# Optimization experiments

Measured on AMD Instinct MI355X. Metric: run time of the kernel, lower is better.

## Reference

```python
import jax, jax.numpy as jnp
import numpy as np

N = 8192      # nodes
D = 256       # feature dim
GAMMA = 10.0
EPS = 1e-6
DIAG_FILL = -1e-6
# std = 0 in DGM.__init__ default -> the normal(mean=0, std=0) noise is exactly zero, so it is omitted.


def _embed(x, W, edges):
    # minimal message-passing embed_f: h = relu(xW + sum_{(s,d) in E} (xW)[s] -> d)
    h = x @ W
    agg = jax.ops.segment_sum(h[edges[0]], edges[1], num_segments=N)
    return jax.nn.relu(h + agg)


def _cdist(x):
    # pairwise euclidean distance, [N, N]
    sq = jnp.sum(x * x, axis=-1)
    d2 = sq[:, None] + sq[None, :] - 2.0 * (x @ x.T)
    return jnp.sqrt(jnp.clip(d2, 0.0))


def _layernorm(z, gamma, beta):
    # scalar-affine LayerNorm with unbiased std (torch x.std default ddof=1)
    mean = jnp.mean(z, axis=-1, keepdims=True)
    std = jnp.std(z, axis=-1, ddof=1, keepdims=True)
    return gamma * (z - mean) / (std + EPS) + beta


def _entmax15(z):
    # 1.5-entmax over last axis (Peters et al. 2019, exact sort-based algorithm)
    z = z / 2.0
    z = z - jnp.max(z, axis=-1, keepdims=True)
    zs = -jnp.sort(-z, axis=-1)                      # descending sort per row
    k = jnp.arange(1, z.shape[-1] + 1, dtype=z.dtype)
    mean = jnp.cumsum(zs, axis=-1) / k
    meansq = jnp.cumsum(zs * zs, axis=-1) / k
    ss = k * (meansq - mean * mean)
    delta = (1.0 - ss) / k
    tau = mean - jnp.sqrt(jnp.clip(delta, 0.0))
    support = jnp.sum(tau <= zs, axis=-1)            # support size per row
    tau_star = jnp.take_along_axis(tau, (support - 1)[..., None], axis=-1)
    p = jnp.clip(z - tau_star, 0.0)
    return p * p


def setup_inputs() -> dict:
    key = jax.random.key(0)
    k1, k2, k3 = jax.random.split(key, 3)
    x = jax.random.normal(k1, (N, D), dtype=jnp.float32)
    edges = jax.random.randint(k2, (2, 262144), 0, N)
    W = jax.random.normal(k3, (D, D), dtype=jnp.float32) * (1.0 / np.sqrt(D))
    gamma = jnp.full((1,), GAMMA, dtype=jnp.float32)
    beta = jnp.zeros((1,), dtype=jnp.float32)
    return {"x": x, "W": W, "gamma": gamma, "beta": beta, "edges": edges}


def reference(x, W, gamma, beta, edges):
    h = _embed(x, W, edges)                          # [N, D]
    probs = -_cdist(h)                               # [N, N]
    zn = _layernorm(probs, gamma, beta)
    idx = jnp.arange(N)
    zn = zn.at[idx, idx].set(DIAG_FILL)              # fill_diagonal_(-1e-6)
    vprobs = _entmax15(zn)                           # [N, N]
    res = (((vprobs + vprobs.T) * 0.5) > 0).astype(jnp.int32)
    logprobs = jnp.sum(res, axis=1)
    # NOTE: torch returns res.nonzero().t_() (data-dependent shape); we return the
    # equivalent dense adjacency `res` to stay jit-compatible.
    return h, res, logprobs
```

## Files before the change

kernel.cpp:

```cpp
#include <hip/hip_runtime.h>

#define N_NODES 8192
#define NMASK 8191
#define DIMF 256
#define LN_EPS 1e-6f
#define DIAG_Z (-5e-7f)
#define QSCALE 256.0f
#define QINV (1.0f / 256.0f)
#define LDA 40
#define WBS 66

typedef float f32x4 __attribute__((ext_vector_type(4)));
typedef unsigned short ushort8v __attribute__((ext_vector_type(8)));
typedef unsigned short ushort4v __attribute__((ext_vector_type(4)));
typedef short short8v __attribute__((ext_vector_type(8)));

__device__ __forceinline__ unsigned short f2bf(float f) {
  unsigned int u = __float_as_uint(f);
  u = (u + 0x7FFFu + ((u >> 16) & 1u)) >> 16;
  return (unsigned short)u;
}
__device__ __forceinline__ float bf2f(unsigned short s) {
  return __uint_as_float(((unsigned int)s) << 16);
}

__global__ void DGM_22857815949798_kernel() {}

__global__ __launch_bounds__(256) void DGM_22857815949798_dtp(const unsigned short* __restrict__ W16,
                                                              int hint, int* __restrict__ flag) {
  __shared__ float red[4];
  const int t = threadIdx.x;
  if (hint == 0 || hint == 1) { if (t == 0) flag[0] = hint; return; }
  float m = 0.f;
  for (int i = t; i < 2048; i += 256) {
    float v = fabsf(bf2f(W16[i]));
    if (!(v < 1e6f)) v = 1e6f;
    m += v;
  }
#pragma unroll
  for (int o = 32; o; o >>= 1) m += __shfl_down(m, o);
  if ((t & 63) == 0) red[t >> 6] = m;
  __syncthreads();
  if (t == 0) flag[0] = ((red[0] + red[1] + red[2] + red[3]) * (1.0f / 2048.0f) < 10.0f) ? 1 : 0;
}

__global__ __launch_bounds__(256) void DGM_22857815949798_init(int* deg, int* cursor) {
  int i = blockIdx.x * 256 + threadIdx.x;
  if (i < N_NODES) { deg[i] = 0; cursor[i] = 0; }
}

__global__ __launch_bounds__(256) void DGM_22857815949798_e1(const void* __restrict__ xv,
                                                             const void* __restrict__ Wv,
                                                             const int* __restrict__ flag,
                                                             float* __restrict__ h0) {
  __shared__ float xs[4][DIMF];
  const int bf = *flag;
  const int t = threadIdx.x;
  const int r0 = blockIdx.x * 4;
#pragma unroll
  for (int r = 0; r < 4; ++r) {
    size_t idx = (size_t)(r0 + r) * DIMF + t;
    xs[r][t] = bf ? bf2f(((const unsigned short*)xv)[idx]) : ((const float*)xv)[idx];
  }
  __syncthreads();
  float a0 = 0.f, a1 = 0.f, a2 = 0.f, a3 = 0.f;
  for (int k = 0; k < DIMF; ++k) {
    size_t wi = (size_t)k * DIMF + t;
    float w = bf ? bf2f(((const unsigned short*)Wv)[wi]) : ((const float*)Wv)[wi];
    a0 = fmaf(xs[0][k], w, a0);
    a1 = fmaf(xs[1][k], w, a1);
    a2 = fmaf(xs[2][k], w, a2);
    a3 = fmaf(xs[3][k], w, a3);
  }
  h0[(size_t)(r0 + 0) * DIMF + t] = a0;
  h0[(size_t)(r0 + 1) * DIMF + t] = a1;
  h0[(size_t)(r0 + 2) * DIMF + t] = a2;
  h0[(size_t)(r0 + 3) * DIMF + t] = a3;
}

__global__ __launch_bounds__(256) void DGM_22857815949798_deg(const int* __restrict__ dst,
                                                              int* __restrict__ deg, int E) {
  int e = blockIdx.x * 256 + threadIdx.x;
  if (e < E) atomicAdd(&deg[dst[e] & NMASK], 1);
}

__global__ __launch_bounds__(256) void DGM_22857815949798_scan(const int* __restrict__ deg,
                                                               int* __restrict__ off) {
  __shared__ int part[256];
  const int t = threadIdx.x;
  const int base = t * 32;
  int loc[32];
  int s = 0;
#pragma unroll
  for (int q = 0; q < 32; ++q) { loc[q] = s; s += deg[base + q]; }
  part[t] = s;
  __syncthreads();
  for (int o = 1; o < 256; o <<= 1) {
    int v = (t >= o) ? part[t - o] : 0;
    __syncthreads();
    part[t] += v;
    __syncthreads();
  }
  int excl = (t == 0) ? 0 : part[t - 1];
#pragma unroll
  for (int q = 0; q < 32; ++q) off[base + q] = excl + loc[q];
  if (t == 255) off[N_NODES] = excl + s;
}

__global__ __launch_bounds__(256) void DGM_22857815949798_scatter(const int* __restrict__ src,
                                                                  const int* __restrict__ dst,
                                                                  const int* __restrict__ off,
                                                                  int* __restrict__ cursor,
                                                                  int* __restrict__ adj, int E) {
  int e = blockIdx.x * 256 + threadIdx.x;
  if (e < E) {
    int d = dst[e] & NMASK;
    int p = atomicAdd(&cursor[d], 1);
    unsigned w = (unsigned)(off[d] + p);
    if (w < (unsigned)E) adj[w] = src[e] & NMASK;
  }
}

__global__ __launch_bounds__(256) void DGM_22857815949798_embed(const float* __restrict__ h0,
                                                                const int* __restrict__ adj,
                                                                const int* __restrict__ off,
                                                                void* __restrict__ hout, int outf,
                                                                unsigned short* __restrict__ hhi,
                                                                unsigned short* __restrict__ hlo,
                                                                float* __restrict__ sq) {
  __shared__ float rbuf[4];
  const int d = blockIdx.x;
  const int c = threadIdx.x;
  const int lane = c & 63, wv = c >> 6;
  int beg = off[d], end = off[d + 1];
  if (beg < 0) beg = 0;
  if (end > 262144) end = 262144;
  float v = h0[(size_t)d * DIMF + c];
  for (int e = beg; e < end; ++e) {
    int s = adj[e] & NMASK;
    v += h0[(size_t)s * DIMF + c];
  }
  v = fmaxf(v, 0.f);
  size_t idx = (size_t)d * DIMF + c;
  float vb;
  if (outf) {
    ((float*)hout)[idx] = v;
    vb = v;
    unsigned int u = __float_as_uint(v);
    unsigned short hi = (unsigned short)(u >> 16);
    hhi[idx] = hi;
    hlo[idx] = f2bf(v - __uint_as_float(u & 0xFFFF0000u));
  } else {
    unsigned short us = f2bf(v);
    ((unsigned short*)hout)[idx] = us;
    vb = bf2f(us);
  }
  float p = vb * vb;
#pragma unroll
  for (int o = 32; o; o >>= 1) p += __shfl_down(p, o);
  if (lane == 0) rbuf[wv] = p;
  __syncthreads();
  if (c == 0) sq[d] = rbuf[0] + rbuf[1] + rbuf[2] + rbuf[3];
}

__global__ __launch_bounds__(256) void DGM_22857815949798_gramq(const unsigned short* __restrict__ hhi,
                                                                const unsigned short* __restrict__ hlo,
                                                                const float* __restrict__ sq,
                                                                unsigned short* __restrict__ dq) {
  __shared__ __align__(16) unsigned short lds[20480];
  unsigned short* Ahi = lds;
  unsigned short* Alo = lds + 5120;
  unsigned short* Bhi = lds + 10240;
  unsigned short* Blo = lds + 15360;
  __shared__ float sqi[128], sqj[128];
  const int t = threadIdx.x;
  const int lane = t & 63, wv = t >> 6;
  const int quad = lane >> 4, cid = lane & 15;

  const int bt = blockIdx.x;
  int bi = (int)((129.0f - sqrtf(129.0f * 129.0f - 8.0f * (float)bt)) * 0.5f);
  if (bi < 0) bi = 0;
  if (bi > 63) bi = 63;
  while (bi * (129 - bi) / 2 > bt) --bi;
  while ((bi + 1) * (128 - bi) / 2 <= bt) ++bi;
  const int bj = bi + (bt - bi * (129 - bi) / 2);
  const int i0 = bi * 128, j0 = bj * 128;

  const int wM = (wv >> 1) * 64, wN = (wv & 1) * 64;
  const int arow = t >> 2;
  const int kcol = (t & 3) * 8;

  if (t < 128) sqi[t] = sq[i0 + t];
  else sqj[t - 128] = sq[j0 + t - 128];

  const size_t aoff = (size_t)(i0 + arow) * DIMF + kcol;
  const size_t boff = (size_t)(j0 + arow) * DIMF + kcol;

  f32x4 acc[4][4] = {};

  for (int ko = 0; ko < 8; ++ko) {
    const int kk = ko * 32;
    ushort8v ah0 = *(const ushort8v*)(hhi + aoff + kk);
    ushort8v ah1 = *(const ushort8v*)(hhi + aoff + (size_t)64 * DIMF + kk);
    ushort8v al0 = *(const ushort8v*)(hlo + aoff + kk);
    ushort8v al1 = *(const ushort8v*)(hlo + aoff + (size_t)64 * DIMF + kk);
    ushort8v bh0 = *(const ushort8v*)(hhi + boff + kk);
    ushort8v bh1 = *(const ushort8v*)(hhi + boff + (size_t)64 * DIMF + kk);
    ushort8v bl0 = *(const ushort8v*)(hlo + boff + kk);
    ushort8v bl1 = *(const ushort8v*)(hlo + boff + (size_t)64 * DIMF + kk);
    __syncthreads();
    *(ushort8v*)(Ahi + arow * LDA + kcol) = ah0;
    *(ushort8v*)(Ahi + (arow + 64) * LDA + kcol) = ah1;
    *(ushort8v*)(Alo + arow * LDA + kcol) = al0;
    *(ushort8v*)(Alo + (arow + 64) * LDA + kcol) = al1;
    *(ushort8v*)(Bhi + arow * LDA + kcol) = bh0;
    *(ushort8v*)(Bhi + (arow + 64) * LDA + kcol) = bh1;
    *(ushort8v*)(Blo + arow * LDA + kcol) = bl0;
    *(ushort8v*)(Blo + (arow + 64) * LDA + kcol) = bl1;
    __syncthreads();

    short8v fah[4], fal[4], fbh[4], fbl[4];
#pragma unroll
    for (int mi = 0; mi < 4; ++mi) {
      const int ro = (wM + mi * 16 + cid) * LDA + quad * 8;
      fah[mi] = *(const short8v*)(Ahi + ro);
      fal[mi] = *(const short8v*)(Alo + ro);
    }
#pragma unroll
    for (int ni = 0; ni < 4; ++ni) {
      const int ro = (wN + ni * 16 + cid) * LDA + quad * 8;
      fbh[ni] = *(const short8v*)(Bhi + ro);
      fbl[ni] = *(const short8v*)(Blo + ro);
    }
#pragma unroll
    for (int mi = 0; mi < 4; ++mi)
#pragma unroll
      for (int ni = 0; ni < 4; ++ni) {
        acc[mi][ni] = __builtin_amdgcn_mfma_f32_16x16x32_bf16(fah[mi], fbh[ni], acc[mi][ni], 0, 0, 0);
        acc[mi][ni] = __builtin_amdgcn_mfma_f32_16x16x32_bf16(fah[mi], fbl[ni], acc[mi][ni], 0, 0, 0);
        acc[mi][ni] = __builtin_amdgcn_mfma_f32_16x16x32_bf16(fal[mi], fbh[ni], acc[mi][ni], 0, 0, 0);
      }
  }
  __syncthreads();

  unsigned short* wbuf = lds + wv * 4224;
#pragma unroll
  for (int mi = 0; mi < 4; ++mi) {
    const int rbase = wM + mi * 16 + quad * 4;
#pragma unroll
    for (int ni = 0; ni < 4; ++ni) {
      const int gj = j0 + wN + ni * 16 + cid;
      const float sj = sqj[wN + ni * 16 + cid];
      ushort4v m4;
#pragma unroll
      for (int r = 0; r < 4; ++r) {
        const int gi = i0 + rbase + r;
        float d2 = sqi[rbase + r] + sj - 2.0f * acc[mi][ni][r];
        float dd = (gi == gj) ? 0.0f : sqrtf(fmaxf(d2, 0.0f));
        int u = (int)(dd * QSCALE + 0.5f);
        u = (u > 65535) ? 65535 : u;
        wbuf[(rbase - wM + r) * WBS + ni * 16 + cid] = (unsigned short)u;
        m4[r] = (unsigned short)u;
      }
      if (bi != bj)
        *(ushort4v*)(dq + (size_t)gj * N_NODES + (i0 + rbase)) = m4;
    }
  }
#pragma unroll
  for (int it = 0; it < 8; ++it) {
    const int row = it * 8 + (lane >> 3);
    const int col = (lane & 7) * 8;
    size_t goff = (size_t)(i0 + wM + row) * N_NODES + (size_t)(j0 + wN + col);
    *(ushort8v*)(dq + goff) = *(const ushort8v*)(wbuf + row * WBS + col);
  }
}

__global__ __launch_bounds__(256) void DGM_22857815949798_gramm(const unsigned short* __restrict__ H,
                                                                const float* __restrict__ sq,
                                                                unsigned short* __restrict__ dq) {
  __shared__ __align__(16) unsigned short lds[16384];
  unsigned short* Alds = lds;
  unsigned short* Blds = lds + 128 * LDA;
  const int t = threadIdx.x;
  const int lane = t & 63, wv = t >> 6;
  const int i0 = blockIdx.y * 128, j0 = blockIdx.x * 128;
  const int wM = (wv >> 1) * 64, wN = (wv & 1) * 64;
  const int quad = lane >> 4, cid = lane & 15;
  const int arow = t >> 2;
  const int kcol = (t & 3) * 8;

  const unsigned short* gA = H + (size_t)(i0 + arow) * DIMF + kcol;
  const unsigned short* gB = H + (size_t)(j0 + arow) * DIMF + kcol;

  f32x4 acc[4][4] = {};

  for (int ko = 0; ko < 8; ++ko) {
    const int kk = ko * 32;
    ushort8v a0 = *(const ushort8v*)(gA + kk);
    ushort8v a1 = *(const ushort8v*)(gA + (size_t)64 * DIMF + kk);
    ushort8v b0 = *(const ushort8v*)(gB + kk);
    ushort8v b1 = *(const ushort8v*)(gB + (size_t)64 * DIMF + kk);
    __syncthreads();
    *(ushort8v*)(Alds + arow * LDA + kcol) = a0;
    *(ushort8v*)(Alds + (arow + 64) * LDA + kcol) = a1;
    *(ushort8v*)(Blds + arow * LDA + kcol) = b0;
    *(ushort8v*)(Blds + (arow + 64) * LDA + kcol) = b1;
    __syncthreads();

    short8v af[4], bq[4];
#pragma unroll
    for (int mi = 0; mi < 4; ++mi)
      af[mi] = *(const short8v*)(Alds + (wM + mi * 16 + cid) * LDA + quad * 8);
#pragma unroll
    for (int ni = 0; ni < 4; ++ni)
      bq[ni] = *(const short8v*)(Blds + (wN + ni * 16 + cid) * LDA + quad * 8);
#pragma unroll
    for (int mi = 0; mi < 4; ++mi)
#pragma unroll
      for (int ni = 0; ni < 4; ++ni)
        acc[mi][ni] = __builtin_amdgcn_mfma_f32_16x16x32_bf16(af[mi], bq[ni], acc[mi][ni], 0, 0, 0);
  }
  __syncthreads();

  unsigned short* wbuf = lds + wv * 4096;
#pragma unroll
  for (int mi = 0; mi < 4; ++mi) {
#pragma unroll
    for (int r = 0; r < 4; ++r) {
      const int lrow = mi * 16 + quad * 4 + r;
      const int gi = i0 + wM + lrow;
      const float si = sq[gi];
#pragma unroll
      for (int ni = 0; ni < 4; ++ni) {
        const int gj = j0 + wN + ni * 16 + cid;
        float d2 = si + sq[gj] - 2.0f * acc[mi][ni][r];
        float dd = (gi == gj) ? 0.0f : sqrtf(fmaxf(d2, 0.0f));
        int u = (int)(dd * QSCALE + 0.5f);
        u = (u > 65535) ? 65535 : u;
        wbuf[lrow * 64 + ni * 16 + cid] = (unsigned short)u;
      }
    }
  }
#pragma unroll
  for (int it = 0; it < 8; ++it) {
    int o = it * 512 + lane * 8;
    int row = o >> 6;
    int col = o & 63;
    size_t goff = (size_t)(i0 + wM + row) * N_NODES + (size_t)(j0 + wN + col);
    *(ushort8v*)(dq + goff) = *(const ushort8v*)(wbuf + o);
  }
}

__global__ __launch_bounds__(256) void DGM_22857815949798_tau(const unsigned short* __restrict__ dq,
                                                              const void* __restrict__ gv,
                                                              const void* __restrict__ bv,
                                                              const int* __restrict__ flag,
                                                              float* __restrict__ dthr,
                                                              float* __restrict__ taug) {
  __shared__ float cand[N_NODES];
  __shared__ int ccount;
  __shared__ float redS[4], redM[4];
  __shared__ float bc[4];
  const int i = blockIdx.x;
  const int t = threadIdx.x;
  const int lane = t & 63, wv = t >> 6;
  const unsigned short* row = dq + (size_t)i * N_NODES;

  float dv[32];
  float sum = 0.f, dmin = 1e30f;
#pragma unroll
  for (int q = 0; q < 4; ++q) {
    const int j0 = q * 2048 + t * 8;
    ushort8v pk = *(const ushort8v*)(row + j0);
#pragma unroll
    for (int e = 0; e < 8; ++e) {
      float d = (float)pk[e] * QINV;
      dv[q * 8 + e] = d;
      sum += d;
      if (j0 + e != i) dmin = fminf(dmin, d);
    }
  }
#pragma unroll
  for (int o = 32; o; o >>= 1) {
    sum += __shfl_down(sum, o);
    dmin = fminf(dmin, __shfl_down(dmin, o));
  }
  if (lane == 0) { redS[wv] = sum; redM[wv] = dmin; }
  __syncthreads();
  if (t == 0) {
    float S = redS[0] + redS[1] + redS[2] + redS[3];
    bc[0] = S * (1.0f / (float)N_NODES);
    bc[1] = fminf(fminf(redM[0], redM[1]), fminf(redM[2], redM[3]));
  }
  __syncthreads();
  const float mean = bc[0];
  float ss = 0.f;
#pragma unroll
  for (int q = 0; q < 32; ++q) { float u = dv[q] - mean; ss += u * u; }
#pragma unroll
  for (int o = 32; o; o >>= 1) ss += __shfl_down(ss, o);
  if (lane == 0) redS[wv] = ss;
  __syncthreads();
  if (t == 0) {
    float Q = redS[0] + redS[1] + redS[2] + redS[3];
    float sd = sqrtf(fmaxf(Q * (1.0f / (float)(N_NODES - 1)), 0.f));
    int bf = *flag;
    float gamma = bf ? bf2f(((const unsigned short*)gv)[0]) : ((const float*)gv)[0];
    float beta = bf ? bf2f(((const unsigned short*)bv)[0]) : ((const float*)bv)[0];
    float a = gamma / (2.0f * (sd + LN_EPS));
    float hb = 0.5f * beta;
    float zmax = fmaxf(a * (mean - bc[1]) + hb, DIAG_Z);
    bc[1] = a; bc[2] = zmax; bc[3] = hb;
    ccount = 0;
  }
  __syncthreads();
  const float a = bc[1], zmax = bc[2], hb = bc[3];
  const float zlo = zmax - 1.0f;
#pragma unroll
  for (int q = 0; q < 4; ++q) {
#pragma unroll
    for (int e = 0; e < 8; ++e) {
      const int j = q * 2048 + t * 8 + e;
      float z = a * (mean - dv[q * 8 + e]) + hb;
      if (j == i) z = DIAG_Z;
      if (z > zlo) {
        int p = atomicAdd(&ccount, 1);
        if (p < N_NODES) cand[p] = z;
      }
    }
  }
  __syncthreads();
  if (wv == 0) {
    const int n = (ccount < N_NODES) ? ccount : N_NODES;
    float lo = zlo, hi = zmax;
    for (int it = 0; it < 30; ++it) {
      float mid = 0.5f * (lo + hi);
      float s = 0.f;
      for (int p = lane; p < n; p += 64) {
        float u = cand[p] - mid;
        s += (u > 0.f) ? u * u : 0.f;
      }
#pragma unroll
      for (int o = 32; o; o >>= 1) s += __shfl_down(s, o);
      s = __shfl(s, 0);
      if (s > 1.f) lo = mid; else hi = mid;
    }
    if (lane == 0) {
      float tau = 0.5f * (lo + hi);
      taug[i] = tau;
      dthr[i] = mean - (tau - hb) / a;
    }
  }
}

__global__ __launch_bounds__(256) void DGM_22857815949798_res(const unsigned short* __restrict__ dq,
                                                              void* __restrict__ Rv, int outf,
                                                              const float* __restrict__ dthr,
                                                              const float* __restrict__ taug,
                                                              void* __restrict__ lp) {
  __shared__ int redc[4];
  const int i = blockIdx.x;
  const int t = threadIdx.x;
  const int lane = t & 63, wv = t >> 6;
  const float di = dthr[i];
  const float ti = taug[i];
  const unsigned short* row = dq + (size_t)i * N_NODES;
  int c = 0;
#pragma unroll
  for (int q = 0; q < 4; ++q) {
    const int j0 = q * 2048 + t * 8;
    const size_t go = (size_t)i * N_NODES + j0;
    ushort8v pk = *(const ushort8v*)(row + j0);
    f32x4 c0 = *(const f32x4*)(dthr + j0);
    f32x4 c1 = *(const f32x4*)(dthr + j0 + 4);
    bool rr[8];
#pragma unroll
    for (int e = 0; e < 8; ++e) {
      float d = (float)pk[e] * QINV;
      float dj = (e < 4) ? c0[e] : c1[e - 4];
      bool r = (d < di) || (d < dj);
      if (j0 + e == i) r = (DIAG_Z > ti);
      rr[e] = r;
      c += r ? 1 : 0;
    }
    if (outf) {
      f32x4 o0, o1;
#pragma unroll
      for (int e = 0; e < 4; ++e) { o0[e] = rr[e] ? 1.0f : 0.0f; o1[e] = rr[e + 4] ? 1.0f : 0.0f; }
      *(f32x4*)((float*)Rv + go) = o0;
      *(f32x4*)((float*)Rv + go + 4) = o1;
    } else {
      ushort8v ob;
#pragma unroll
      for (int e = 0; e < 8; ++e) ob[e] = rr[e] ? (unsigned short)0x3F80 : (unsigned short)0;
      *(ushort8v*)((unsigned short*)Rv + go) = ob;
    }
  }
#pragma unroll
  for (int o = 32; o; o >>= 1) c += __shfl_down(c, o);
  if (lane == 0) redc[wv] = c;
  __syncthreads();
  if (t == 0) {
    int tot = redc[0] + redc[1] + redc[2] + redc[3];
    if (outf) ((float*)lp)[i] = (float)tot;
    else ((unsigned short*)lp)[i] = f2bf((float)tot);
  }
}

static bool DGM_rng(const void* p, void** start, size_t* sz) {
  void* st = nullptr;
  size_t s = 0;
  if (hipPointerGetAttribute(&st, HIP_POINTER_ATTRIBUTE_RANGE_START_ADDR,
                             (hipDeviceptr_t)p) != hipSuccess) return false;
  if (hipPointerGetAttribute(&s, HIP_POINTER_ATTRIBUTE_RANGE_SIZE,
                             (hipDeviceptr_t)p) != hipSuccess) return false;
  *start = st; *sz = s;
  return true;
}
static bool DGM_exactish(size_t s, size_t x) { return s >= x && s < x + (size_t)(2u << 20); }

extern "C" int kernel_launch(void* const* d_in, const int* in_sizes, int n_in,
                             void* d_out, int out_size, void* d_ws, size_t ws_size,
                             hipStream_t stream) {
  (void)n_in; (void)out_size; (void)ws_size;

  int curdev = 0;
  (void)hipGetDevice(&curdev);
  int tgtdev = curdev;
  hipPointerAttribute_t pa;
  if (hipPointerGetAttributes(&pa, d_out) == hipSuccess) {
    if (pa.device >= 0 && pa.device < 64) tgtdev = pa.device;
  }
  if (tgtdev != curdev) (void)hipSetDevice(tgtdev);

  hipStreamCaptureStatus cap = hipStreamCaptureStatusNone;
  hipError_t se = hipStreamIsCapturing(stream, &cap);
  const bool validStream = (se == hipSuccess);
  const bool capturing = validStream && (cap != hipStreamCaptureStatusNone);
  hipStream_t s = validStream ? stream : (hipStream_t)0;

  const size_t OUT_B16 = 134238208ull;
  const size_t OUT_B32 = 268476416ull;
  void* outp = d_out;
  void* wsp = d_ws;
  int outf = 0;
  {
    void* st3 = nullptr; size_t s3 = 0; bool ok3 = DGM_rng(d_out, &st3, &s3);
    void* st5 = nullptr; size_t s5 = 0; bool ok5 = DGM_rng(d_ws, &st5, &s5);
    if (ok3 && st3 == d_out && DGM_exactish(s3, OUT_B16)) { outp = d_out; wsp = d_ws; outf = 0; }
    else if (ok3 && st3 == d_out && DGM_exactish(s3, OUT_B32)) { outp = d_out; wsp = d_ws; outf = 1; }
    else if (ok5 && st5 == d_ws && DGM_exactish(s5, OUT_B16)) { outp = d_ws; wsp = d_out; outf = 0; }
    else if (ok5 && st5 == d_ws && DGM_exactish(s5, OUT_B32)) { outp = d_ws; wsp = d_out; outf = 1; }
    else if (ok3 && s3 >= (200u << 20)) { outf = 1; }
  }

  int hint = -1;
  {
    void* stx = nullptr; size_t sx = 0;
    if (DGM_rng(d_in[0], &stx, &sx) && stx == d_in[0]) {
      if (DGM_exactish(sx, 4194304ull)) hint = 1;
      else if (DGM_exactish(sx, 8388608ull)) hint = 0;
    }
  }

  int E = in_sizes[4] / 2;
  if (E <= 0 || E > 8388608) E = 262144;
  const int* edges = (const int*)d_in[4];
  const int* esrc = edges;
  const int* edst = edges + E;

  const size_t esz = outf ? 4 : 2;
  char* ob = (char*)outp;
  void* h_area = ob;
  void* res_area = ob + (size_t)N_NODES * DIMF * esz;
  void* lp_area = ob + ((size_t)N_NODES * DIMF + (size_t)N_NODES * N_NODES) * esz;

  char* R = (char*)res_area;
  float* h0 = (float*)R;
  int* adj = (int*)(R + 8u * 1024 * 1024);
  int* deg = (int*)(R + 9u * 1024 * 1024);
  int* cursor = (int*)(R + 9u * 1024 * 1024 + 32768);
  int* off = (int*)(R + 9u * 1024 * 1024 + 65536);

  char* wb = (char*)wsp;
  int* flag = (int*)wb;
  float* sq = (float*)(wb + 4096);
  float* dthr = (float*)(wb + 4096 + 32768);
  float* taug = (float*)(wb + 4096 + 65536);
  unsigned short* hhi = (unsigned short*)(wb + (1u << 20));
  unsigned short* hlo = (unsigned short*)(wb + (1u << 20) + (4u << 20));
  unsigned short* dq16 = (unsigned short*)(wb + (16u << 20));

  (void)hipGetLastError();

  DGM_22857815949798_dtp<<<1, 256, 0, s>>>((const unsigned short*)d_in[1], hint, flag);
  DGM_22857815949798_init<<<N_NODES / 256, 256, 0, s>>>(deg, cursor);
  DGM_22857815949798_e1<<<N_NODES / 4, 256, 0, s>>>(d_in[0], d_in[1], flag, h0);
  DGM_22857815949798_deg<<<(E + 255) / 256, 256, 0, s>>>(edst, deg, E);
  DGM_22857815949798_scan<<<1, 256, 0, s>>>(deg, off);
  DGM_22857815949798_scatter<<<(E + 255) / 256, 256, 0, s>>>(esrc, edst, off, cursor, adj, E);
  DGM_22857815949798_embed<<<N_NODES, 256, 0, s>>>(h0, adj, off, h_area, outf, hhi, hlo, sq);
  if (outf) {
    DGM_22857815949798_gramq<<<2080, 256, 0, s>>>(hhi, hlo, sq, dq16);
  } else {
    dim3 gg(N_NODES / 128, N_NODES / 128);
    DGM_22857815949798_gramm<<<gg, 256, 0, s>>>((const unsigned short*)h_area, sq, dq16);
  }
  DGM_22857815949798_tau<<<N_NODES, 256, 0, s>>>(dq16, d_in[2], d_in[3], flag, dthr, taug);
  DGM_22857815949798_res<<<N_NODES, 256, 0, s>>>(dq16, res_area, outf, dthr, taug, lp_area);

  hipError_t err = hipGetLastError();
  if (!capturing) {
    if (err != hipSuccess) {
      (void)hipDeviceSynchronize();
      (void)hipGetLastError();
    }
    (void)hipStreamSynchronize(s);
  }

  if (tgtdev != curdev) (void)hipSetDevice(curdev);
  return 0;
}

extern "C" int launch(void* const* a, const int* b, int c, void* d, int e, void* f,
                      size_t g, hipStream_t h) { return kernel_launch(a, b, c, d, e, f, g, h); }
extern "C" int run(void* const* a, const int* b, int c, void* d, int e, void* f,
                   size_t g, hipStream_t h) { return kernel_launch(a, b, c, d, e, f, g, h); }
extern "C" int kernel_main(void* const* a, const int* b, int c, void* d, int e, void* f,
                           size_t g, hipStream_t h) { return kernel_launch(a, b, c, d, e, f, g, h); }
extern "C" int DGM_22857815949798(void* const* a, const int* b, int c, void* d, int e, void* f,
                                  size_t g, hipStream_t h) { return kernel_launch(a, b, c, d, e, f, g, h); }
```

Before: 653.7 us.

## Use direct global-to-LDS loads in gram kernel and fuse init kernels

The gram tile loads now use global_load_lds to move hi/lo bf16 tiles straight from global memory into LDS, skipping the register staging. The LDS layout drops the padded stride in favour of a dense 32-element row to match the per-lane 16-byte placement. The dtype-probe and degree/cursor init kernels are merged into one launch to save a kernel launch. The unpadded layout can bring back LDS bank conflicts on the fragment reads, and the early return inside block 0 now sits after the init stores.

```diff
diff --git a/kernel.cpp b/kernel.cpp
--- a/kernel.cpp
+++ b/kernel.cpp
@@ -15,6 +15,9 @@
 typedef unsigned short ushort4v __attribute__((ext_vector_type(4)));
 typedef short short8v __attribute__((ext_vector_type(8)));
 
+typedef const __attribute__((address_space(1))) unsigned int* gas_t;
+typedef __attribute__((address_space(3))) unsigned int* las_t;
+
 __device__ __forceinline__ unsigned short f2bf(float f) {
   unsigned int u = __float_as_uint(f);
   u = (u + 0x7FFFu + ((u >> 16) & 1u)) >> 16;
@@ -26,27 +29,28 @@
 
 __global__ void DGM_22857815949798_kernel() {}
 
-__global__ __launch_bounds__(256) void DGM_22857815949798_dtp(const unsigned short* __restrict__ W16,
-                                                              int hint, int* __restrict__ flag) {
-  __shared__ float red[4];
-  const int t = threadIdx.x;
-  if (hint == 0 || hint == 1) { if (t == 0) flag[0] = hint; return; }
-  float m = 0.f;
-  for (int i = t; i < 2048; i += 256) {
-    float v = fabsf(bf2f(W16[i]));
-    if (!(v < 1e6f)) v = 1e6f;
-    m += v;
-  }
-#pragma unroll
-  for (int o = 32; o; o >>= 1) m += __shfl_down(m, o);
-  if ((t & 63) == 0) red[t >> 6] = m;
-  __syncthreads();
-  if (t == 0) flag[0] = ((red[0] + red[1] + red[2] + red[3]) * (1.0f / 2048.0f) < 10.0f) ? 1 : 0;
-}
-
-__global__ __launch_bounds__(256) void DGM_22857815949798_init(int* deg, int* cursor) {
+__global__ __launch_bounds__(256) void DGM_22857815949798_dtpi(const unsigned short* __restrict__ W16,
+                                                               int hint, int* __restrict__ flag,
+                                                               int* __restrict__ deg,
+                                                               int* __restrict__ cursor) {
   int i = blockIdx.x * 256 + threadIdx.x;
   if (i < N_NODES) { deg[i] = 0; cursor[i] = 0; }
+  if (blockIdx.x == 0) {
+    __shared__ float red[4];
+    const int t = threadIdx.x;
+    if (hint == 0 || hint == 1) { if (t == 0) flag[0] = hint; return; }
+    float m = 0.f;
+    for (int k = t; k < 2048; k += 256) {
+      float v = fabsf(bf2f(W16[k]));
+      if (!(v < 1e6f)) v = 1e6f;
+      m += v;
+    }
+#pragma unroll
+    for (int o = 32; o; o >>= 1) m += __shfl_down(m, o);
+    if ((t & 63) == 0) red[t >> 6] = m;
+    __syncthreads();
+    if (t == 0) flag[0] = ((red[0] + red[1] + red[2] + red[3]) * (1.0f / 2048.0f) < 10.0f) ? 1 : 0;
+  }
 }
 
 __global__ __launch_bounds__(256) void DGM_22857815949798_e1(const void* __restrict__ xv,
@@ -147,8 +151,7 @@
     ((float*)hout)[idx] = v;
     vb = v;
     unsigned int u = __float_as_uint(v);
-    unsigned short hi = (unsigned short)(u >> 16);
-    hhi[idx] = hi;
+    hhi[idx] = (unsigned short)(u >> 16);
     hlo[idx] = f2bf(v - __uint_as_float(u & 0xFFFF0000u));
   } else {
     unsigned short us = f2bf(v);
@@ -167,11 +170,11 @@
                                                                 const unsigned short* __restrict__ hlo,
                                                                 const float* __restrict__ sq,
                                                                 unsigned short* __restrict__ dq) {
-  __shared__ __align__(16) unsigned short lds[20480];
+  __shared__ __align__(16) unsigned short lds[17408];
   unsigned short* Ahi = lds;
-  unsigned short* Alo = lds + 5120;
-  unsigned short* Bhi = lds + 10240;
-  unsigned short* Blo = lds + 15360;
+  unsigned short* Alo = lds + 4096;
+  unsigned short* Bhi = lds + 8192;
+  unsigned short* Blo = lds + 12288;
   __shared__ float sqi[128], sqj[128];
   const int t = threadIdx.x;
   const int lane = t & 63, wv = t >> 6;
@@ -195,40 +198,42 @@
 
   const size_t aoff = (size_t)(i0 + arow) * DIMF + kcol;
   const size_t boff = (size_t)(j0 + arow) * DIMF + kcol;
+  const size_t aoff2 = aoff + (size_t)64 * DIMF;
+  const size_t boff2 = boff + (size_t)64 * DIMF;
+  unsigned short* dA0 = Ahi + t * 8;
+  unsigned short* dA1 = Ahi + 2048 + t * 8;
+  unsigned short* dAl0 = Alo + t * 8;
+  unsigned short* dAl1 = Alo + 2048 + t * 8;
+  unsigned short* dB0 = Bhi + t * 8;
+  unsigned short* dB1 = Bhi + 2048 + t * 8;
+  unsigned short* dBl0 = Blo + t * 8;
+  unsigned short* dBl1 = Blo + 2048 + t * 8;
 
   f32x4 acc[4][4] = {};
 
   for (int ko = 0; ko < 8; ++ko) {
     const int kk = ko * 32;
-    ushort8v ah0 = *(const ushort8v*)(hhi + aoff + kk);
-    ushort8v ah1 = *(const ushort8v*)(hhi + aoff + (size_t)64 * DIMF + kk);
-    ushort8v al0 = *(const ushort8v*)(hlo + aoff + kk);
-    ushort8v al1 = *(const ushort8v*)(hlo + aoff + (size_t)64 * DIMF + kk);
-    ushort8v bh0 = *(const ushort8v*)(hhi + boff + kk);
-    ushort8v bh1 = *(const ushort8v*)(hhi + boff + (size_t)64 * DIMF + kk);
-    ushort8v bl0 = *(const ushort8v*)(hlo + boff + kk);
-    ushort8v bl1 = *(const ushort8v*)(hlo + boff + (size_t)64 * DIMF + kk);
     __syncthreads();
-    *(ushort8v*)(Ahi + arow * LDA + kcol) = ah0;
-    *(ushort8v*)(Ahi + (arow + 64) * LDA + kcol) = ah1;
-    *(ushort8v*)(Alo + arow * LDA + kcol) = al0;
-    *(ushort8v*)(Alo + (arow + 64) * LDA + kcol) = al1;
-    *(ushort8v*)(Bhi + arow * LDA + kcol) = bh0;
-    *(ushort8v*)(Bhi + (arow + 64) * LDA + kcol) = bh1;
-    *(ushort8v*)(Blo + arow * LDA + kcol) = bl0;
-    *(ushort8v*)(Blo + (arow + 64) * LDA + kcol) = bl1;
+    __builtin_amdgcn_global_load_lds((gas_t)(const void*)(hhi + aoff + kk), (las_t)(void*)dA0, 16, 0, 0);
+    __builtin_amdgcn_global_load_lds((gas_t)(const void*)(hhi + aoff2 + kk), (las_t)(void*)dA1, 16, 0, 0);
+    __builtin_amdgcn_global_load_lds((gas_t)(const void*)(hlo + aoff + kk), (las_t)(void*)dAl0, 16, 0, 0);
+    __builtin_amdgcn_global_load_lds((gas_t)(const void*)(hlo + aoff2 + kk), (las_t)(void*)dAl1, 16, 0, 0);
+    __builtin_amdgcn_global_load_lds((gas_t)(const void*)(hhi + boff + kk), (las_t)(void*)dB0, 16, 0, 0);
+    __builtin_amdgcn_global_load_lds((gas_t)(const void*)(hhi + boff2 + kk), (las_t)(void*)dB1, 16, 0, 0);
+    __builtin_amdgcn_global_load_lds((gas_t)(const void*)(hlo + boff + kk), (las_t)(void*)dBl0, 16, 0, 0);
+    __builtin_amdgcn_global_load_lds((gas_t)(const void*)(hlo + boff2 + kk), (las_t)(void*)dBl1, 16, 0, 0);
     __syncthreads();
 
     short8v fah[4], fal[4], fbh[4], fbl[4];
 #pragma unroll
     for (int mi = 0; mi < 4; ++mi) {
-      const int ro = (wM + mi * 16 + cid) * LDA + quad * 8;
+      const int ro = (wM + mi * 16 + cid) * 32 + quad * 8;
       fah[mi] = *(const short8v*)(Ahi + ro);
       fal[mi] = *(const short8v*)(Alo + ro);
     }
 #pragma unroll
     for (int ni = 0; ni < 4; ++ni) {
-      const int ro = (wN + ni * 16 + cid) * LDA + quad * 8;
+      const int ro = (wN + ni * 16 + cid) * 32 + quad * 8;
       fbh[ni] = *(const short8v*)(Bhi + ro);
       fbl[ni] = *(const short8v*)(Blo + ro);
     }
@@ -593,8 +598,7 @@
 
   (void)hipGetLastError();
 
-  DGM_22857815949798_dtp<<<1, 256, 0, s>>>((const unsigned short*)d_in[1], hint, flag);
-  DGM_22857815949798_init<<<N_NODES / 256, 256, 0, s>>>(deg, cursor);
+  DGM_22857815949798_dtpi<<<32, 256, 0, s>>>((const unsigned short*)d_in[1], hint, flag, deg, cursor);
   DGM_22857815949798_e1<<<N_NODES / 4, 256, 0, s>>>(d_in[0], d_in[1], flag, h0);
   DGM_22857815949798_deg<<<(E + 255) / 256, 256, 0, s>>>(edst, deg, E);
   DGM_22857815949798_scan<<<1, 256, 0, s>>>(deg, off);
```

Result: no change. 647.1 us (-1.0%).
